# Performance work log

Measured on AMD Instinct MI355X. Metric: run time of the kernel, lower is better.

The kernel has to match this reference:

```python
import jax, jax.numpy as jnp
import numpy as np

MAX_DISP = 4  # PWC-Net correlation: displacements in [-4,4] -> 9x9 = 81 channels


def setup_inputs() -> dict:
    key = jax.random.key(0)
    k1, k2 = jax.random.split(key)
    B, C, H, W = 8, 128, 112, 192
    tensorFirst = jax.random.normal(k1, (B, C, H, W), dtype=jnp.float32)
    tensorSecond = jax.random.normal(k2, (B, C, H, W), dtype=jnp.float32)
    return {"tensorFirst": tensorFirst, "tensorSecond": tensorSecond}


def reference(tensorFirst, tensorSecond):
    B, C, H, W = tensorFirst.shape
    D = MAX_DISP
    # zero-pad second by max displacement on each spatial side (rbot padding of 8 = 2*4)
    padded = jnp.pad(tensorSecond, ((0, 0), (0, 0), (D, D), (D, D)))
    outs = []
    # fixed 9x9 displacement grid; channel index = (dy+4)*9 + (dx+4)
    for dy in range(2 * D + 1):
        for dx in range(2 * D + 1):
            shifted = jax.lax.dynamic_slice(padded, (0, 0, dy, dx), (B, C, H, W))
            # dot product over channels, normalized by C (sumelems in the cupy kernel)
            outs.append(jnp.mean(tensorFirst * shifted, axis=1))
    return jnp.stack(outs, axis=1)  # [B, 81, H, W]
```

## Files before the change

kernel.cpp:

```cpp
#include <hip/hip_runtime.h>


namespace {
constexpr int kC = 128;
constexpr int kH = 112;
constexpr int kW = 192;
constexpr int kD = 4;
constexpr int kKD = 9;
constexpr int kHW = kH * kW;
constexpr long long kCHW = (long long)kC * kHW;

constexpr int PX = 8;
constexpr int XG = kW / PX;
constexpr int YT = 8;
constexpr int NT = XG * YT;
}

__device__ __attribute__((aligned(16))) float g_zeros[4] = {0.f, 0.f, 0.f, 0.f};

__global__ __launch_bounds__(NT, 4)
void corr81_kernel(const float* __restrict__ first,
                   const float* __restrict__ second,
                   float* __restrict__ out) {
  const int g = blockIdx.x;
  const int b = g & 7;
  const int i = g >> 3;
  const int dy = i % kKD;
  const int y0 = (i / kKD) * YT;

  const int tid = threadIdx.x;
  const int xg = tid % XG;
  const int yl = tid / XG;
  const int px0 = xg * PX;
  const int y = y0 + yl;
  const int ys = y + dy - kD;

  float acc[PX][kKD];
#pragma unroll
  for (int p = 0; p < PX; ++p)
#pragma unroll
    for (int d = 0; d < kKD; ++d) acc[p][d] = 0.0f;

  if ((unsigned)ys < (unsigned)kH) {
    const bool left = (xg == 0);
    const bool right = (xg == XG - 1);

    const float* fp = first + (long long)b * kCHW + (long long)y * kW + px0;
    const float* sp = second + (long long)b * kCHW + (long long)ys * kW + px0;
    const float* pw0 = left ? g_zeros : (sp - 4);
    const float* pw3 = right ? g_zeros : (sp + 8);
    const long long st0 = left ? 0 : kHW;
    const long long st3 = right ? 0 : kHW;

    for (int c = 0; c < kC; ++c) {
      const float4 f0 = *(const float4*)(fp);
      const float4 f1 = *(const float4*)(fp + 4);
      const float4 w0 = *(const float4*)(pw0);
      const float4 w1 = *(const float4*)(sp);
      const float4 w2 = *(const float4*)(sp + 4);
      const float4 w3 = *(const float4*)(pw3);

      const float fa[PX] = {f0.x, f0.y, f0.z, f0.w, f1.x, f1.y, f1.z, f1.w};
      const float sw[16] = {w0.x, w0.y, w0.z, w0.w, w1.x, w1.y, w1.z, w1.w,
                            w2.x, w2.y, w2.z, w2.w, w3.x, w3.y, w3.z, w3.w};
#pragma unroll
      for (int p = 0; p < PX; ++p)
#pragma unroll
        for (int d = 0; d < kKD; ++d)
          acc[p][d] = fmaf(fa[p], sw[p + d], acc[p][d]);

      fp += kHW;
      sp += kHW;
      pw0 += st0;
      pw3 += st3;
    }
  }

  const float scale = 1.0f / (float)kC;
  float* obase = out + ((long long)b * 81 + (long long)dy * kKD) * kHW +
                 (long long)y * kW + px0;
#pragma unroll
  for (int d = 0; d < kKD; ++d) {
    float4 o0 = make_float4(acc[0][d] * scale, acc[1][d] * scale,
                            acc[2][d] * scale, acc[3][d] * scale);
    float4 o1 = make_float4(acc[4][d] * scale, acc[5][d] * scale,
                            acc[6][d] * scale, acc[7][d] * scale);
    float* op = obase + (long long)d * kHW;
    *(float4*)op = o0;
    *(float4*)(op + 4) = o1;
  }
}

extern "C" void kernel_launch(void* const* d_in, const int* in_sizes, int n_in,
                              void* d_out, int out_size, void* d_ws, size_t ws_size,
                              hipStream_t stream) {
  const float* first = (const float*)d_in[0];
  const float* second = (const float*)d_in[1];
  float* out = (float*)d_out;

  const int grid = 8 * (kH / YT) * kKD;
  corr81_kernel<<<grid, NT, 0, stream>>>(first, second, out);
}
```

Baseline: 331.6 us.

## Stage per-channel input tiles in LDS with double-buffered async global_load_lds

Each block now loads its 8-row tiles of both inputs for one channel into shared memory using the global_load_lds DMA builtin. The copies are double buffered so the next channel loads while the current one is computed. Threads then read their pixels and the neighbouring halo from LDS instead of issuing overlapping global float4 loads, and out-of-range rows point at a zero row in global memory. The aim is to cut redundant global/L1 traffic and hide load latency. The cost is two block barriers per channel pair, extra LDS use, and FMAs now run on rows that fall outside the image.

```diff
diff --git a/kernel.cpp b/kernel.cpp
--- a/kernel.cpp
+++ b/kernel.cpp
@@ -14,14 +14,26 @@
 constexpr int XG = kW / PX;
 constexpr int YT = 8;
 constexpr int NT = XG * YT;
+constexpr int TILE = YT * kW;
 }
 
-__device__ __attribute__((aligned(16))) float g_zeros[4] = {0.f, 0.f, 0.f, 0.f};
+__device__ __attribute__((aligned(16))) float g_zero_row[kW] = {};
+
+typedef const __attribute__((address_space(1))) void* gas_ptr;
+typedef __attribute__((address_space(3))) void* las_ptr;
+
+__device__ __forceinline__ void gload16(const float* g, float* l) {
+  __builtin_amdgcn_global_load_lds((gas_ptr)g, (las_ptr)l, 16, 0, 0);
+}
 
 __global__ __launch_bounds__(NT, 4)
 void corr81_kernel(const float* __restrict__ first,
                    const float* __restrict__ second,
                    float* __restrict__ out) {
+  __shared__ __align__(16) float zpad[4];
+  __shared__ __align__(16) float Sb[2][TILE];
+  __shared__ __align__(16) float Fb[2][TILE];
+
   const int g = blockIdx.x;
   const int b = g & 7;
   const int i = g >> 3;
@@ -32,8 +44,25 @@
   const int xg = tid % XG;
   const int yl = tid / XG;
   const int px0 = xg * PX;
-  const int y = y0 + yl;
-  const int ys = y + dy - kD;
+  const int ys0 = y0 + dy - kD;
+
+  if (tid == 0) { zpad[0] = 0.f; zpad[1] = 0.f; zpad[2] = 0.f; zpad[3] = 0.f; }
+
+  const float* fsrc = first + (long long)b * kCHW + (long long)y0 * kW +
+                      (long long)tid * 4;
+  const float* ssrc[2];
+  long long sstr[2];
+#pragma unroll
+  for (int j = 0; j < 2; ++j) {
+    const int pos = j * NT + tid;
+    const int r = pos / 48;
+    const int col4 = (pos - r * 48) * 4;
+    const int ysr = ys0 + r;
+    const bool inb = (unsigned)ysr < (unsigned)kH;
+    ssrc[j] = inb ? (second + (long long)b * kCHW + (long long)ysr * kW + col4)
+                  : (g_zero_row + col4);
+    sstr[j] = inb ? (long long)kHW : 0ll;
+  }
 
   float acc[PX][kKD];
 #pragma unroll
@@ -41,44 +70,52 @@
 #pragma unroll
     for (int d = 0; d < kKD; ++d) acc[p][d] = 0.0f;
 
-  if ((unsigned)ys < (unsigned)kH) {
-    const bool left = (xg == 0);
-    const bool right = (xg == XG - 1);
+  auto stage = [&](int P) {
+    gload16(fsrc,            &Fb[P][tid * 4]);
+    gload16(fsrc + NT * 4,   &Fb[P][tid * 4 + NT * 4]);
+    gload16(ssrc[0],         &Sb[P][tid * 4]);
+    gload16(ssrc[1],         &Sb[P][tid * 4 + NT * 4]);
+    fsrc += kHW;
+    ssrc[0] += sstr[0];
+    ssrc[1] += sstr[1];
+  };
 
-    const float* fp = first + (long long)b * kCHW + (long long)y * kW + px0;
-    const float* sp = second + (long long)b * kCHW + (long long)ys * kW + px0;
-    const float* pw0 = left ? g_zeros : (sp - 4);
-    const float* pw3 = right ? g_zeros : (sp + 8);
-    const long long st0 = left ? 0 : kHW;
-    const long long st3 = right ? 0 : kHW;
+  auto compute = [&](int P) {
+    const float* fp = &Fb[P][yl * kW + px0];
+    const float* s1 = &Sb[P][yl * kW + px0];
+    const float* w0p = (xg == 0) ? zpad : (s1 - 4);
+    const float* w3p = (xg == XG - 1) ? zpad : (s1 + 8);
+    const float4 f0 = *(const float4*)(fp);
+    const float4 f1 = *(const float4*)(fp + 4);
+    const float4 w0 = *(const float4*)(w0p);
+    const float4 w1 = *(const float4*)(s1);
+    const float4 w2 = *(const float4*)(s1 + 4);
+    const float4 w3 = *(const float4*)(w3p);
 
-    for (int c = 0; c < kC; ++c) {
-      const float4 f0 = *(const float4*)(fp);
-      const float4 f1 = *(const float4*)(fp + 4);
-      const float4 w0 = *(const float4*)(pw0);
-      const float4 w1 = *(const float4*)(sp);
-      const float4 w2 = *(const float4*)(sp + 4);
-      const float4 w3 = *(const float4*)(pw3);
+    const float fa[PX] = {f0.x, f0.y, f0.z, f0.w, f1.x, f1.y, f1.z, f1.w};
+    const float sw[16] = {w0.x, w0.y, w0.z, w0.w, w1.x, w1.y, w1.z, w1.w,
+                          w2.x, w2.y, w2.z, w2.w, w3.x, w3.y, w3.z, w3.w};
+#pragma unroll
+    for (int p = 0; p < PX; ++p)
+#pragma unroll
+      for (int d = 0; d < kKD; ++d)
+        acc[p][d] = fmaf(fa[p], sw[p + d], acc[p][d]);
+  };
 
-      const float fa[PX] = {f0.x, f0.y, f0.z, f0.w, f1.x, f1.y, f1.z, f1.w};
-      const float sw[16] = {w0.x, w0.y, w0.z, w0.w, w1.x, w1.y, w1.z, w1.w,
-                            w2.x, w2.y, w2.z, w2.w, w3.x, w3.y, w3.z, w3.w};
-#pragma unroll
-      for (int p = 0; p < PX; ++p)
-#pragma unroll
-        for (int d = 0; d < kKD; ++d)
-          acc[p][d] = fmaf(fa[p], sw[p + d], acc[p][d]);
-
-      fp += kHW;
-      sp += kHW;
-      pw0 += st0;
-      pw3 += st3;
-    }
+  stage(0);
+  __syncthreads();
+  for (int c = 0; c < kC; c += 2) {
+    stage(1);
+    compute(0);
+    __syncthreads();
+    if (c + 2 < kC) stage(0);
+    compute(1);
+    __syncthreads();
   }
 
   const float scale = 1.0f / (float)kC;
   float* obase = out + ((long long)b * 81 + (long long)dy * kKD) * kHW +
-                 (long long)y * kW + px0;
+                 (long long)(y0 + yl) * kW + px0;
 #pragma unroll
   for (int d = 0; d < kKD; ++d) {
     float4 o0 = make_float4(acc[0][d] * scale, acc[1][d] * scale,
```

Result: faster. 283.5 us (-14.5%).
